# Kernel tuning notes

Measured on AMD Instinct MI355X. Metric: run time of the kernel, lower is better.

The kernel has to match this reference:

```python
import jax, jax.numpy as jnp
import numpy as np

B = 65536
NUM_INPUTS = 256
NUM_HIDDEN = 256


def setup_inputs() -> dict:
    key = jax.random.key(0)
    ks = jax.random.split(key, 11)
    f32 = jnp.float32
    return {
        "x": jax.random.normal(ks[0], (B, NUM_INPUTS), dtype=f32),
        "h_t_1": jax.random.normal(ks[1], (B, NUM_HIDDEN), dtype=f32),
        "Wz": jax.random.normal(ks[2], (NUM_INPUTS, NUM_HIDDEN), dtype=f32),
        "Uz": jax.random.normal(ks[3], (NUM_HIDDEN, NUM_HIDDEN), dtype=f32),
        "bz": jax.random.normal(ks[4], (NUM_HIDDEN,), dtype=f32),
        "Wr": jax.random.normal(ks[5], (NUM_INPUTS, NUM_HIDDEN), dtype=f32),
        "Ur": jax.random.normal(ks[6], (NUM_HIDDEN, NUM_HIDDEN), dtype=f32),
        "br": jax.random.normal(ks[7], (NUM_HIDDEN,), dtype=f32),
        "Wh": jax.random.normal(ks[8], (NUM_INPUTS, NUM_HIDDEN), dtype=f32),
        "Uh": jax.random.normal(ks[9], (NUM_HIDDEN, NUM_HIDDEN), dtype=f32),
        "bh": jax.random.normal(ks[10], (NUM_HIDDEN,), dtype=f32),
    }


def reference(x, h_t_1, Wz, Uz, bz, Wr, Ur, br, Wh, Uh, bh):
    # update gate z = sigmoid(x@Wz + h@Uz + bz)
    z = jax.nn.sigmoid(x @ Wz + h_t_1 @ Uz + bz)
    # reset gate r = sigmoid(x@Wr + h@Ur + br)
    r = jax.nn.sigmoid(x @ Wr + h_t_1 @ Ur + br)
    # candidate: tanh(x@Wh + (r*h)@Uh + bh)
    h_hat = jnp.tanh(x @ Wh + (r * h_t_1) @ Uh + bh)
    h_t = z * h_t_1 + (1.0 - z) * h_hat
    return (h_t, h_t)
```

## Files before the change

kernel.cpp:

```cpp
#include <hip/hip_runtime.h>
#include <hip/hip_fp16.h>


#define NHID 256
#define B_ROWS 65536
#define MT 64
#define RT 4
#define CPW 2
#define GATE_STRIDE (16 * 16 * 64 * 8)

typedef _Float16 half8 __attribute__((ext_vector_type(8)));
typedef _Float16 half4_t __attribute__((ext_vector_type(4)));
typedef _Float16 half2_t __attribute__((ext_vector_type(2)));
typedef float floatx4 __attribute__((ext_vector_type(4)));

__device__ __forceinline__ int lidx(int m, int c) {
    return m * 256 + ((((c >> 3) ^ (m & 7)) << 3)) + (c & 7);
}

__device__ __forceinline__ void barrier_lgkm() {
    __builtin_amdgcn_sched_barrier(0);
    asm volatile("s_waitcnt lgkmcnt(0)" ::: "memory");
    __builtin_amdgcn_s_barrier();
    __builtin_amdgcn_sched_barrier(0);
}

__global__ __launch_bounds__(256) void pack_weights_kernel(
    const float* __restrict__ Wz, const float* __restrict__ Uz,
    const float* __restrict__ Wr, const float* __restrict__ Ur,
    const float* __restrict__ Wh, const float* __restrict__ Uh,
    _Float16* __restrict__ packed)
{
    int tid = blockIdx.x * blockDim.x + threadIdx.x;
    int lane = tid & 63;
    int s    = (tid >> 6) & 15;
    int ct   = (tid >> 10) & 15;
    int g    = tid >> 14;
    const float* W = (g == 0) ? Wz : (g == 1) ? Wr : Wh;
    const float* U = (g == 0) ? Uz : (g == 1) ? Ur : Uh;
    int n  = ct * 16 + (lane & 15);
    int k0 = s * 32 + (lane >> 4) * 8;
    half8 v;
#pragma unroll
    for (int j = 0; j < 8; ++j) {
        int k = k0 + j;
        float f = (k < 256) ? W[k * 256 + n] : U[(k - 256) * 256 + n];
        v[j] = (_Float16)f;
    }
    *reinterpret_cast<half8*>(packed + (size_t)tid * 8) = v;
}

#define WFRAG(base, ct, s) \
    (*reinterpret_cast<const half8*>((base) + (size_t)((((ct) * 16 + (s)) * 64 + lane) * 8)))

__global__ __launch_bounds__(512, 4) void gru_main_kernel(
    const float* __restrict__ x, const float* __restrict__ h,
    const _Float16* __restrict__ wpack,
    const float* __restrict__ bz, const float* __restrict__ br,
    const float* __restrict__ bh,
    float* __restrict__ out)
{
    __shared__ __align__(16) _Float16 lsm[MT * 256 * 2];
    _Float16* lx = lsm;
    _Float16* lh = lsm + MT * 256;

    const int tid  = threadIdx.x;
    const int lane = tid & 63;
    const int wave = tid >> 6;
    const int row0 = blockIdx.x * MT;
    const int m_lo = lane & 15;
    const int quad = lane >> 4;
    const int mx   = m_lo & 7;
    const int ct0  = wave * CPW;

    const _Float16* wz = wpack;
    const _Float16* wr = wpack + GATE_STRIDE;
    const _Float16* wh = wpack + 2 * GATE_STRIDE;

    half8 wzb[2][CPW], wrb[2][CPW];
    wzb[0][0] = WFRAG(wz, ct0 + 0, 0);
    wzb[0][1] = WFRAG(wz, ct0 + 1, 0);
    wrb[0][0] = WFRAG(wr, ct0 + 0, 0);
    wrb[0][1] = WFRAG(wr, ct0 + 1, 0);

    {
        const float4* xv = reinterpret_cast<const float4*>(x + (size_t)row0 * NHID);
        const float4* hv = reinterpret_cast<const float4*>(h + (size_t)row0 * NHID);
#pragma unroll
        for (int it = 0; it < (MT * 64) / 512; ++it) {
            int i = it * 512 + tid;
            int m = i >> 6;
            int c = (i & 63) * 4;
            float4 a = xv[i];
            float4 b = hv[i];
            half4_t va = { (_Float16)a.x, (_Float16)a.y, (_Float16)a.z, (_Float16)a.w };
            half4_t vb = { (_Float16)b.x, (_Float16)b.y, (_Float16)b.z, (_Float16)b.w };
            *reinterpret_cast<half4_t*>(&lx[lidx(m, c)]) = va;
            *reinterpret_cast<half4_t*>(&lh[lidx(m, c)]) = vb;
        }
    }
    barrier_lgkm();

    half2_t zpk[CPW][RT][4];

    floatx4 accz[CPW][RT];
    floatx4 accr[CPW][RT];
#pragma unroll
    for (int c = 0; c < CPW; ++c)
#pragma unroll
        for (int rt = 0; rt < RT; ++rt) {
            accz[c][rt] = (floatx4){0.f, 0.f, 0.f, 0.f};
            accr[c][rt] = (floatx4){0.f, 0.f, 0.f, 0.f};
        }

#pragma unroll
    for (int s = 0; s < 16; ++s) {
        const int cur = s & 1, nxt = cur ^ 1;
        if (s < 15) {
            wzb[nxt][0] = WFRAG(wz, ct0 + 0, s + 1);
            wzb[nxt][1] = WFRAG(wz, ct0 + 1, s + 1);
            wrb[nxt][0] = WFRAG(wr, ct0 + 0, s + 1);
            wrb[nxt][1] = WFRAG(wr, ct0 + 1, s + 1);
        }
        const _Float16* asrc = (s < 8) ? lx : lh;
        const int kcx = (((s & 7) * 4 + quad) ^ mx) << 3;
        half8 af[RT];
#pragma unroll
        for (int rt = 0; rt < RT; ++rt)
            af[rt] = *reinterpret_cast<const half8*>(&asrc[(rt * 16 + m_lo) * 256 + kcx]);
        __builtin_amdgcn_s_setprio(1);
#pragma unroll
        for (int c = 0; c < CPW; ++c)
#pragma unroll
            for (int rt = 0; rt < RT; ++rt) {
                accz[c][rt] = __builtin_amdgcn_mfma_f32_16x16x32_f16(af[rt], wzb[cur][c], accz[c][rt], 0, 0, 0);
                accr[c][rt] = __builtin_amdgcn_mfma_f32_16x16x32_f16(af[rt], wrb[cur][c], accr[c][rt], 0, 0, 0);
            }
        __builtin_amdgcn_s_setprio(0);
    }

    half8 whb[2][CPW];
    whb[0][0] = WFRAG(wh, ct0 + 0, 0);
    whb[0][1] = WFRAG(wh, ct0 + 1, 0);
    float bzv[CPW], brv[CPW], bhv[CPW];
#pragma unroll
    for (int c = 0; c < CPW; ++c) {
        const int col = (ct0 + c) * 16 + m_lo;
        bzv[c] = bz[col];
        brv[c] = br[col];
        bhv[c] = bh[col];
    }

    barrier_lgkm();

#pragma unroll
    for (int c = 0; c < CPW; ++c) {
        const int col = (ct0 + c) * 16 + m_lo;
#pragma unroll
        for (int rt = 0; rt < RT; ++rt) {
#pragma unroll
            for (int e = 0; e < 4; ++e) {
                const int row = rt * 16 + quad * 4 + e;
                float sz = accz[c][rt][e] + bzv[c];
                float sr = accr[c][rt][e] + brv[c];
                float zv = 1.f / (1.f + __expf(-sz));
                float rv = 1.f / (1.f + __expf(-sr));
                const int li = lidx(row, col);
                float hval = (float)lh[li];
                lh[li] = (_Float16)(rv * hval);
                zpk[c][rt][e] = half2_t{ (_Float16)(zv * hval), (_Float16)(1.f - zv) };
            }
        }
    }

    barrier_lgkm();

    floatx4 acch[CPW][RT];
#pragma unroll
    for (int c = 0; c < CPW; ++c)
#pragma unroll
        for (int rt = 0; rt < RT; ++rt)
            acch[c][rt] = (floatx4){0.f, 0.f, 0.f, 0.f};

#pragma unroll
    for (int s = 0; s < 16; ++s) {
        const int cur = s & 1, nxt = cur ^ 1;
        if (s < 15) {
            whb[nxt][0] = WFRAG(wh, ct0 + 0, s + 1);
            whb[nxt][1] = WFRAG(wh, ct0 + 1, s + 1);
        }
        const _Float16* asrc = (s < 8) ? lx : lh;
        const int kcx = (((s & 7) * 4 + quad) ^ mx) << 3;
        half8 af[RT];
#pragma unroll
        for (int rt = 0; rt < RT; ++rt)
            af[rt] = *reinterpret_cast<const half8*>(&asrc[(rt * 16 + m_lo) * 256 + kcx]);
        __builtin_amdgcn_s_setprio(1);
#pragma unroll
        for (int c = 0; c < CPW; ++c)
#pragma unroll
            for (int rt = 0; rt < RT; ++rt)
                acch[c][rt] = __builtin_amdgcn_mfma_f32_16x16x32_f16(af[rt], whb[cur][c], acch[c][rt], 0, 0, 0);
        __builtin_amdgcn_s_setprio(0);
    }

    const size_t OUT2 = (size_t)B_ROWS * NHID;
#pragma unroll
    for (int c = 0; c < CPW; ++c) {
        const int col = (ct0 + c) * 16 + m_lo;
#pragma unroll
        for (int rt = 0; rt < RT; ++rt) {
#pragma unroll
            for (int e = 0; e < 4; ++e) {
                const int row = rt * 16 + quad * 4 + e;
                float sh = acch[c][rt][e] + bhv[c];
                float e2 = __expf(2.f * sh);
                float hh = 1.f - 2.f / (e2 + 1.f);
                float zh  = (float)zpk[c][rt][e][0];
                float omz = (float)zpk[c][rt][e][1];
                float ht  = zh + omz * hh;
                size_t idx = (size_t)(row0 + row) * NHID + col;
                __builtin_nontemporal_store(ht, &out[idx]);
                __builtin_nontemporal_store(ht, &out[OUT2 + idx]);
            }
        }
    }
}

extern "C" void kernel_launch(void* const* d_in, const int* in_sizes, int n_in,
                              void* d_out, int out_size, void* d_ws, size_t ws_size,
                              hipStream_t stream) {
    (void)in_sizes; (void)n_in; (void)out_size; (void)ws_size;
    const float* x  = (const float*)d_in[0];
    const float* h  = (const float*)d_in[1];
    const float* Wz = (const float*)d_in[2];
    const float* Uz = (const float*)d_in[3];
    const float* bz = (const float*)d_in[4];
    const float* Wr = (const float*)d_in[5];
    const float* Ur = (const float*)d_in[6];
    const float* br = (const float*)d_in[7];
    const float* Wh = (const float*)d_in[8];
    const float* Uh = (const float*)d_in[9];
    const float* bh = (const float*)d_in[10];
    float* out = (float*)d_out;
    _Float16* wpack = (_Float16*)d_ws;

    pack_weights_kernel<<<192, 256, 0, stream>>>(Wz, Uz, Wr, Ur, Wh, Uh, wpack);
    gru_main_kernel<<<B_ROWS / MT, 512, 0, stream>>>(x, h, wpack, bz, br, bh, out);
}
```

Baseline: 319.6 us.

## Halve row tile and split z/r gate GEMMs into sequential passes

The row tile drops from 64 to 32, and the fused z/r GEMM loop becomes two passes that reuse one accumulator and one weight buffer. This cuts register and shared-memory pressure so more blocks fit per CU. The candidate GEMM puts a barrier between its x half and its h half, so the x half overlaps the r*h LDS update, and bias loads move ahead of the first barrier. In exchange, each weight fragment is reused over half as many rows, so weight traffic from L2 doubles, and there are more passes over the LDS A fragments.

```diff
diff --git a/kernel.cpp b/kernel.cpp
--- a/kernel.cpp
+++ b/kernel.cpp
@@ -4,8 +4,8 @@
 
 #define NHID 256
 #define B_ROWS 65536
-#define MT 64
-#define RT 4
+#define MT 32
+#define RT 2
 #define CPW 2
 #define GATE_STRIDE (16 * 16 * 64 * 8)
 
@@ -77,11 +77,18 @@
     const _Float16* wr = wpack + GATE_STRIDE;
     const _Float16* wh = wpack + 2 * GATE_STRIDE;
 
-    half8 wzb[2][CPW], wrb[2][CPW];
-    wzb[0][0] = WFRAG(wz, ct0 + 0, 0);
-    wzb[0][1] = WFRAG(wz, ct0 + 1, 0);
-    wrb[0][0] = WFRAG(wr, ct0 + 0, 0);
-    wrb[0][1] = WFRAG(wr, ct0 + 1, 0);
+    half8 wb[2][CPW];
+    wb[0][0] = WFRAG(wz, ct0 + 0, 0);
+    wb[0][1] = WFRAG(wz, ct0 + 1, 0);
+
+    float bzv[CPW], brv[CPW], bhv[CPW];
+#pragma unroll
+    for (int c = 0; c < CPW; ++c) {
+        const int col = (ct0 + c) * 16 + m_lo;
+        bzv[c] = bz[col];
+        brv[c] = br[col];
+        bhv[c] = bh[col];
+    }
 
     {
         const float4* xv = reinterpret_cast<const float4*>(x + (size_t)row0 * NHID);
@@ -101,129 +108,147 @@
     }
     barrier_lgkm();
 
-    half2_t zpk[CPW][RT][4];
-
-    floatx4 accz[CPW][RT];
-    floatx4 accr[CPW][RT];
-#pragma unroll
-    for (int c = 0; c < CPW; ++c)
-#pragma unroll
-        for (int rt = 0; rt < RT; ++rt) {
-            accz[c][rt] = (floatx4){0.f, 0.f, 0.f, 0.f};
-            accr[c][rt] = (floatx4){0.f, 0.f, 0.f, 0.f};
-        }
+    floatx4 acc[CPW][RT];
+
+#pragma unroll
+    for (int c = 0; c < CPW; ++c)
+#pragma unroll
+        for (int rt = 0; rt < RT; ++rt)
+            acc[c][rt] = (floatx4){0.f, 0.f, 0.f, 0.f};
 
 #pragma unroll
     for (int s = 0; s < 16; ++s) {
-        const int cur = s & 1, nxt = cur ^ 1;
-        if (s < 15) {
-            wzb[nxt][0] = WFRAG(wz, ct0 + 0, s + 1);
-            wzb[nxt][1] = WFRAG(wz, ct0 + 1, s + 1);
-            wrb[nxt][0] = WFRAG(wr, ct0 + 0, s + 1);
-            wrb[nxt][1] = WFRAG(wr, ct0 + 1, s + 1);
-        }
         const _Float16* asrc = (s < 8) ? lx : lh;
         const int kcx = (((s & 7) * 4 + quad) ^ mx) << 3;
         half8 af[RT];
 #pragma unroll
         for (int rt = 0; rt < RT; ++rt)
             af[rt] = *reinterpret_cast<const half8*>(&asrc[(rt * 16 + m_lo) * 256 + kcx]);
+        if (s < 15) {
+            wb[(s + 1) & 1][0] = WFRAG(wz, ct0 + 0, s + 1);
+            wb[(s + 1) & 1][1] = WFRAG(wz, ct0 + 1, s + 1);
+        } else {
+            wb[0][0] = WFRAG(wr, ct0 + 0, 0);
+            wb[0][1] = WFRAG(wr, ct0 + 1, 0);
+        }
         __builtin_amdgcn_s_setprio(1);
 #pragma unroll
         for (int c = 0; c < CPW; ++c)
 #pragma unroll
-            for (int rt = 0; rt < RT; ++rt) {
-                accz[c][rt] = __builtin_amdgcn_mfma_f32_16x16x32_f16(af[rt], wzb[cur][c], accz[c][rt], 0, 0, 0);
-                accr[c][rt] = __builtin_amdgcn_mfma_f32_16x16x32_f16(af[rt], wrb[cur][c], accr[c][rt], 0, 0, 0);
+            for (int rt = 0; rt < RT; ++rt)
+                acc[c][rt] = __builtin_amdgcn_mfma_f32_16x16x32_f16(af[rt], wb[s & 1][c], acc[c][rt], 0, 0, 0);
+        __builtin_amdgcn_s_setprio(0);
+    }
+
+    half2_t zreg[CPW][RT][2];
+#pragma unroll
+    for (int c = 0; c < CPW; ++c)
+#pragma unroll
+        for (int rt = 0; rt < RT; ++rt)
+#pragma unroll
+            for (int e = 0; e < 4; ++e) {
+                float sz = acc[c][rt][e] + bzv[c];
+                float zv = 1.f / (1.f + __expf(-sz));
+                zreg[c][rt][e >> 1][e & 1] = (_Float16)zv;
             }
-        __builtin_amdgcn_s_setprio(0);
-    }
-
-    half8 whb[2][CPW];
-    whb[0][0] = WFRAG(wh, ct0 + 0, 0);
-    whb[0][1] = WFRAG(wh, ct0 + 1, 0);
-    float bzv[CPW], brv[CPW], bhv[CPW];
-#pragma unroll
-    for (int c = 0; c < CPW; ++c) {
-        const int col = (ct0 + c) * 16 + m_lo;
-        bzv[c] = bz[col];
-        brv[c] = br[col];
-        bhv[c] = bh[col];
-    }
-
-    barrier_lgkm();
-
-#pragma unroll
-    for (int c = 0; c < CPW; ++c) {
-        const int col = (ct0 + c) * 16 + m_lo;
-#pragma unroll
-        for (int rt = 0; rt < RT; ++rt) {
-#pragma unroll
-            for (int e = 0; e < 4; ++e) {
-                const int row = rt * 16 + quad * 4 + e;
-                float sz = accz[c][rt][e] + bzv[c];
-                float sr = accr[c][rt][e] + brv[c];
-                float zv = 1.f / (1.f + __expf(-sz));
-                float rv = 1.f / (1.f + __expf(-sr));
-                const int li = lidx(row, col);
-                float hval = (float)lh[li];
-                lh[li] = (_Float16)(rv * hval);
-                zpk[c][rt][e] = half2_t{ (_Float16)(zv * hval), (_Float16)(1.f - zv) };
-            }
-        }
-    }
-
-    barrier_lgkm();
-
-    floatx4 acch[CPW][RT];
-#pragma unroll
-    for (int c = 0; c < CPW; ++c)
-#pragma unroll
-        for (int rt = 0; rt < RT; ++rt)
-            acch[c][rt] = (floatx4){0.f, 0.f, 0.f, 0.f};
+
+#pragma unroll
+    for (int c = 0; c < CPW; ++c)
+#pragma unroll
+        for (int rt = 0; rt < RT; ++rt)
+            acc[c][rt] = (floatx4){0.f, 0.f, 0.f, 0.f};
 
 #pragma unroll
     for (int s = 0; s < 16; ++s) {
-        const int cur = s & 1, nxt = cur ^ 1;
-        if (s < 15) {
-            whb[nxt][0] = WFRAG(wh, ct0 + 0, s + 1);
-            whb[nxt][1] = WFRAG(wh, ct0 + 1, s + 1);
-        }
         const _Float16* asrc = (s < 8) ? lx : lh;
         const int kcx = (((s & 7) * 4 + quad) ^ mx) << 3;
         half8 af[RT];
 #pragma unroll
         for (int rt = 0; rt < RT; ++rt)
             af[rt] = *reinterpret_cast<const half8*>(&asrc[(rt * 16 + m_lo) * 256 + kcx]);
+        if (s < 15) {
+            wb[(s + 1) & 1][0] = WFRAG(wr, ct0 + 0, s + 1);
+            wb[(s + 1) & 1][1] = WFRAG(wr, ct0 + 1, s + 1);
+        } else {
+            wb[0][0] = WFRAG(wh, ct0 + 0, 0);
+            wb[0][1] = WFRAG(wh, ct0 + 1, 0);
+        }
         __builtin_amdgcn_s_setprio(1);
 #pragma unroll
         for (int c = 0; c < CPW; ++c)
 #pragma unroll
             for (int rt = 0; rt < RT; ++rt)
-                acch[c][rt] = __builtin_amdgcn_mfma_f32_16x16x32_f16(af[rt], whb[cur][c], acch[c][rt], 0, 0, 0);
+                acc[c][rt] = __builtin_amdgcn_mfma_f32_16x16x32_f16(af[rt], wb[s & 1][c], acc[c][rt], 0, 0, 0);
         __builtin_amdgcn_s_setprio(0);
     }
 
-    const size_t OUT2 = (size_t)B_ROWS * NHID;
+    barrier_lgkm();
+
+    half2_t hreg[CPW][RT][2];
 #pragma unroll
     for (int c = 0; c < CPW; ++c) {
         const int col = (ct0 + c) * 16 + m_lo;
 #pragma unroll
-        for (int rt = 0; rt < RT; ++rt) {
+        for (int rt = 0; rt < RT; ++rt)
 #pragma unroll
             for (int e = 0; e < 4; ++e) {
                 const int row = rt * 16 + quad * 4 + e;
-                float sh = acch[c][rt][e] + bhv[c];
+                float sr = acc[c][rt][e] + brv[c];
+                float rv = 1.f / (1.f + __expf(-sr));
+                const int li = lidx(row, col);
+                _Float16 hval = lh[li];
+                lh[li] = (_Float16)(rv * (float)hval);
+                hreg[c][rt][e >> 1][e & 1] = hval;
+            }
+    }
+
+#pragma unroll
+    for (int c = 0; c < CPW; ++c)
+#pragma unroll
+        for (int rt = 0; rt < RT; ++rt)
+            acc[c][rt] = (floatx4){0.f, 0.f, 0.f, 0.f};
+
+#pragma unroll
+    for (int s = 0; s < 16; ++s) {
+        if (s == 8) barrier_lgkm();
+        const _Float16* asrc = (s < 8) ? lx : lh;
+        const int kcx = (((s & 7) * 4 + quad) ^ mx) << 3;
+        half8 af[RT];
+#pragma unroll
+        for (int rt = 0; rt < RT; ++rt)
+            af[rt] = *reinterpret_cast<const half8*>(&asrc[(rt * 16 + m_lo) * 256 + kcx]);
+        if (s < 15) {
+            wb[(s + 1) & 1][0] = WFRAG(wh, ct0 + 0, s + 1);
+            wb[(s + 1) & 1][1] = WFRAG(wh, ct0 + 1, s + 1);
+        }
+        __builtin_amdgcn_s_setprio(1);
+#pragma unroll
+        for (int c = 0; c < CPW; ++c)
+#pragma unroll
+            for (int rt = 0; rt < RT; ++rt)
+                acc[c][rt] = __builtin_amdgcn_mfma_f32_16x16x32_f16(af[rt], wb[s & 1][c], acc[c][rt], 0, 0, 0);
+        __builtin_amdgcn_s_setprio(0);
+    }
+
+    const size_t OUT2 = (size_t)B_ROWS * NHID;
+#pragma unroll
+    for (int c = 0; c < CPW; ++c) {
+        const int col = (ct0 + c) * 16 + m_lo;
+#pragma unroll
+        for (int rt = 0; rt < RT; ++rt)
+#pragma unroll
+            for (int e = 0; e < 4; ++e) {
+                const int row = rt * 16 + quad * 4 + e;
+                float sh = acc[c][rt][e] + bhv[c];
                 float e2 = __expf(2.f * sh);
                 float hh = 1.f - 2.f / (e2 + 1.f);
-                float zh  = (float)zpk[c][rt][e][0];
-                float omz = (float)zpk[c][rt][e][1];
-                float ht  = zh + omz * hh;
+                float zf = (float)zreg[c][rt][e >> 1][e & 1];
+                float hf = (float)hreg[c][rt][e >> 1][e & 1];
+                float ht = zf * hf + (1.f - zf) * hh;
                 size_t idx = (size_t)(row0 + row) * NHID + col;
                 __builtin_nontemporal_store(ht, &out[idx]);
                 __builtin_nontemporal_store(ht, &out[OUT2 + idx]);
             }
-        }
     }
 }
 
```

Measured after the change: 303.2 us. -5.1%, faster.
